# Kernel optimization log

Hardware: AMD Instinct MI355X
Metric: run time of the kernel (lower is better)

Reference implementation:

```python
import jax, jax.numpy as jnp
import numpy as np

D_IN = 768
D_OUT = 768
NUM_HEADS = 12
HEAD_DIM = D_OUT // NUM_HEADS


def setup_inputs() -> dict:
    key = jax.random.key(0)
    ks = jax.random.split(key, 6)
    s = 0.02
    x = jax.random.normal(ks[0], (4, 1024, D_IN), dtype=jnp.float32)
    # torch Linear weights are [out_features, in_features]
    Wq = jax.random.normal(ks[1], (D_OUT, D_IN), dtype=jnp.float32) * s
    Wk = jax.random.normal(ks[2], (D_OUT, D_IN), dtype=jnp.float32) * s
    Wv = jax.random.normal(ks[3], (D_OUT, D_IN), dtype=jnp.float32) * s
    Wo = jax.random.normal(ks[4], (D_OUT, D_OUT), dtype=jnp.float32) * s
    bo = jax.random.normal(ks[5], (D_OUT,), dtype=jnp.float32) * s
    return {"x": x, "Wq": Wq, "Wk": Wk, "Wv": Wv, "Wo": Wo, "bo": bo}


def reference(x, Wq, Wk, Wv, Wo, bo):
    B, T, _ = x.shape
    H, Dh = NUM_HEADS, HEAD_DIM
    # QKV projections (no bias), reshape to [B, H, T, Dh]
    q = (x @ Wq.T).reshape(B, T, H, Dh).transpose(0, 2, 1, 3)
    k = (x @ Wk.T).reshape(B, T, H, Dh).transpose(0, 2, 1, 3)
    v = (x @ Wv.T).reshape(B, T, H, Dh).transpose(0, 2, 1, 3)
    # Scores [B, H, T, T]. NOTE: original torch code's masked_fill and dropout
    # are not in-place / not assigned, so neither affects the output.
    scores = jnp.einsum("bhqd,bhkd->bhqk", q, k)
    attn = jax.nn.softmax(scores / np.sqrt(Dh).astype(np.float32), axis=-1)
    ctx = jnp.einsum("bhqk,bhkd->bhqd", attn, v)
    ctx = ctx.transpose(0, 2, 1, 3).reshape(B, T, H * Dh)
    return ctx @ Wo.T + bo
```

## Files before the change

kernel.cpp:

```cpp
#include <hip/hip_runtime.h>

typedef _Float16 half8 __attribute__((ext_vector_type(8)));
typedef float f32x4 __attribute__((ext_vector_type(4)));
typedef unsigned short u16;

#define NHEAD 12
#define DHEAD 64
#define DM    768
#define TSEQ  1024
#define LOG2E 1.44269504f

static constexpr size_t OFF_XH  = 0;
static constexpr size_t OFF_WQH = 3145728;
static constexpr size_t OFF_WKH = 3735552;
static constexpr size_t OFF_WVH = 4325376;
static constexpr size_t OFF_WOH = 4915200;
static constexpr size_t OFF_Q   = 5505024;
static constexpr size_t OFF_K   = 8650752;
static constexpr size_t OFF_VT  = 11796480;
static constexpr size_t OFF_CTX = 0;
static constexpr size_t OFF_OP  = 14942208;
static constexpr size_t OFF_ML_BYTES = 42467328;
static constexpr size_t WS_NEED_SPLITK = 43253760;

typedef const __attribute__((address_space(1))) void* gas_ptr;
typedef __attribute__((address_space(3))) void* las_ptr;
__device__ __forceinline__ void gload16(const _Float16* g, _Float16* l) {
    __builtin_amdgcn_global_load_lds((gas_ptr)g, (las_ptr)l, 16, 0, 0);
}

template <int CTRL>
__device__ __forceinline__ float dpp_rotf(float x) {
    int r = __builtin_amdgcn_update_dpp(0, __builtin_bit_cast(int, x), CTRL, 0xF, 0xF, true);
    return __builtin_bit_cast(float, r);
}
__device__ __forceinline__ float row16_max(float x) {
    x = fmaxf(x, dpp_rotf<0x121>(x));
    x = fmaxf(x, dpp_rotf<0x122>(x));
    x = fmaxf(x, dpp_rotf<0x124>(x));
    x = fmaxf(x, dpp_rotf<0x128>(x));
    return x;
}
__device__ __forceinline__ float row16_add(float x) {
    x = x + dpp_rotf<0x121>(x);
    x = x + dpp_rotf<0x122>(x);
    x = x + dpp_rotf<0x124>(x);
    x = x + dpp_rotf<0x128>(x);
    return x;
}

__global__ void cvt_kernel(const float* __restrict__ x, const float* __restrict__ wq,
                           const float* __restrict__ wk, const float* __restrict__ wv,
                           const float* __restrict__ wo, _Float16* __restrict__ ws) {
    int i = (blockIdx.x * 256 + threadIdx.x) * 8;
    const float* src;
    if (i < 3145728)      src = x  + i;
    else if (i < 3735552) src = wq + (i - 3145728);
    else if (i < 4325376) src = wk + (i - 3735552);
    else if (i < 4915200) src = wv + (i - 4325376);
    else                  src = wo + (i - 4915200);
    float4 v0 = *(const float4*)(src);
    float4 v1 = *(const float4*)(src + 4);
    half8 o;
    o[0] = (_Float16)v0.x; o[1] = (_Float16)v0.y;
    o[2] = (_Float16)v0.z; o[3] = (_Float16)v0.w;
    o[4] = (_Float16)v1.x; o[5] = (_Float16)v1.y;
    o[6] = (_Float16)v1.z; o[7] = (_Float16)v1.w;
    *(half8*)(ws + i) = o;
}

__global__ __launch_bounds__(256) void qkv_kernel(_Float16* __restrict__ ws) {
    __shared__ __align__(16) _Float16 ldsA[2][128 * 64];
    __shared__ __align__(16) _Float16 ldsB[2][128 * 64];

    const int z = blockIdx.z;
    const _Float16* __restrict__ xh = ws + OFF_XH;
    const _Float16* __restrict__ w  = ws + (z == 0 ? OFF_WQH : z == 1 ? OFF_WKH : OFF_WVH);
    _Float16* __restrict__ outp     = ws + (z == 0 ? OFF_Q   : z == 1 ? OFF_K   : OFF_VT);

    const int tid  = threadIdx.x;
    const int lane = tid & 63;
    const int wid  = tid >> 6;
    const int quad = lane >> 4, l15 = lane & 15;
    const int wm = (wid & 1) * 64, wn = (wid >> 1) * 64;

    int mb, nb;
    const _Float16 *gA, *gB;
    if (z < 2) {
        mb = blockIdx.x * 128;
        nb = blockIdx.y * 128;
        gA = xh + (size_t)mb * DM;
        gB = w  + (size_t)nb * DM;
    } else {
        mb = blockIdx.y * 128;
        nb = blockIdx.x * 128;
        gA = w  + (size_t)mb * DM;
        gB = xh + (size_t)nb * DM;
    }

    const int srow = tid >> 3;
    const int scol = (((tid & 7) ^ (srow & 7)) * 8);

    auto stage = [&](int buf, int k0) {
#pragma unroll
        for (int c = 0; c < 4; c++) {
            gload16(gA + (size_t)(c * 32 + srow) * DM + scol + k0, &ldsA[buf][c * 2048 + wid * 512]);
            gload16(gB + (size_t)(c * 32 + srow) * DM + scol + k0, &ldsB[buf][c * 2048 + wid * 512]);
        }
    };

    f32x4 acc[4][4] = {};
    stage(0, 0);
    __syncthreads();
    int cur = 0;
    for (int k0 = 0; k0 < DM; k0 += 64) {
        if (k0 + 64 < DM) stage(cur ^ 1, k0 + 64);
        const _Float16* lA = ldsA[cur];
        const _Float16* lB = ldsB[cur];
#pragma unroll
        for (int ks = 0; ks < 2; ks++) {
            half8 a[4], b[4];
#pragma unroll
            for (int t = 0; t < 4; t++) {
                const int phys = (((ks * 4 + quad) ^ (l15 & 7)) * 8);
                a[t] = *(const half8*)(lA + (wm + t * 16 + l15) * 64 + phys);
                b[t] = *(const half8*)(lB + (wn + t * 16 + l15) * 64 + phys);
            }
#pragma unroll
            for (int mt = 0; mt < 4; mt++)
#pragma unroll
                for (int nt = 0; nt < 4; nt++)
                    acc[mt][nt] = __builtin_amdgcn_mfma_f32_16x16x32_f16(a[mt], b[nt], acc[mt][nt], 0, 0, 0);
        }
        __syncthreads();
        cur ^= 1;
    }

#pragma unroll
    for (int mt = 0; mt < 4; mt++)
#pragma unroll
        for (int nt = 0; nt < 4; nt++)
#pragma unroll
            for (int r = 0; r < 4; r++) {
                int m = mb + wm + mt * 16 + quad * 4 + r;
                int n = nb + wn + nt * 16 + l15;
                size_t idx;
                if (z < 2) {
                    int bb = m >> 10, tt = m & 1023;
                    int h = n >> 6, d = n & 63;
                    idx = ((size_t)(bb * NHEAD + h) * TSEQ + tt) * DHEAD + d;
                } else {
                    int h = m >> 6, d = m & 63;
                    int bb = n >> 10, tt = n & 1023;
                    idx = ((size_t)(bb * NHEAD + h) * DHEAD + d) * TSEQ + tt;
                }
                outp[idx] = (_Float16)acc[mt][nt][r];
            }
}

template <int NZ>
__device__ __forceinline__ void attn_body(_Float16* __restrict__ ws) {
    __shared__ __align__(16) _Float16 ldsK[64 * 64];
    __shared__ __align__(16) _Float16 ldsV[64 * 64];
    __shared__ __align__(16) _Float16 ldsP[4][16 * 72];

    const int tid  = threadIdx.x;
    const int lane = tid & 63;
    const int wid  = tid >> 6;
    const int quad = lane >> 4, l15 = lane & 15;
    const int bh = blockIdx.y;
    const int z  = (NZ > 1) ? blockIdx.z : 0;
    const int q0 = blockIdx.x * 64 + wid * 16;
    const int kbeg = z * (TSEQ / NZ), kend = kbeg + TSEQ / NZ;

    const _Float16* __restrict__ Q  = ws + OFF_Q  + (size_t)bh * TSEQ * DHEAD;
    const _Float16* __restrict__ K  = ws + OFF_K  + (size_t)bh * TSEQ * DHEAD;
    const _Float16* __restrict__ VT = ws + OFF_VT + (size_t)bh * DHEAD * TSEQ;
    _Float16* pbase = ldsP[wid];

    const int srow0 = tid >> 3, sc0 = tid & 7;
    const int ldsOff0 = srow0 * 64 + ((sc0 ^ (srow0 & 7)) * 8);
    const int ldsOff1 = (srow0 + 32) * 64 + ((sc0 ^ (srow0 & 7)) * 8);

    half8 qf[2];
#pragma unroll
    for (int ks = 0; ks < 2; ks++) {
        qf[ks] = *(const half8*)(Q + (size_t)(q0 + l15) * DHEAD + ks * 32 + quad * 8);
        qf[ks] = qf[ks] * (_Float16)0.125f;
    }

    float mrun[4], lrun[4];
    f32x4 oacc[4] = {};
#pragma unroll
    for (int r = 0; r < 4; r++) { mrun[r] = -1e30f; lrun[r] = 0.f; }

    uint4 ka, kb, va, vb;
    ka = *(const uint4*)(K + kbeg * DHEAD + tid * 8);
    kb = *(const uint4*)(K + kbeg * DHEAD + 2048 + tid * 8);
    va = *(const uint4*)(VT + (size_t)srow0 * TSEQ + kbeg + sc0 * 8);
    vb = *(const uint4*)(VT + (size_t)(srow0 + 32) * TSEQ + kbeg + sc0 * 8);

    for (int kt = kbeg; kt < kend; kt += 64) {
        *(uint4*)(ldsK + ldsOff0) = ka;
        *(uint4*)(ldsK + ldsOff1) = kb;
        *(uint4*)(ldsV + ldsOff0) = va;
        *(uint4*)(ldsV + ldsOff1) = vb;
        __syncthreads();

        if (kt + 64 < kend) {
            ka = *(const uint4*)(K + (kt + 64) * DHEAD + tid * 8);
            kb = *(const uint4*)(K + (kt + 64) * DHEAD + 2048 + tid * 8);
            va = *(const uint4*)(VT + (size_t)srow0 * TSEQ + kt + 64 + sc0 * 8);
            vb = *(const uint4*)(VT + (size_t)(srow0 + 32) * TSEQ + kt + 64 + sc0 * 8);
        }

        half8 kf[4][2];
#pragma unroll
        for (int n = 0; n < 4; n++)
#pragma unroll
            for (int ks = 0; ks < 2; ks++) {
                int row = n * 16 + l15;
                int phys = (ks * 4 + quad) ^ (row & 7);
                kf[n][ks] = *(const half8*)(ldsK + row * 64 + phys * 8);
            }

        f32x4 s[4] = {};
#pragma unroll
        for (int n = 0; n < 4; n++)
#pragma unroll
            for (int ks = 0; ks < 2; ks++)
                s[n] = __builtin_amdgcn_mfma_f32_16x16x32_f16(qf[ks], kf[n][ks], s[n], 0, 0, 0);

        float tm[4];
#pragma unroll
        for (int r = 0; r < 4; r++) {
            float t = fmaxf(fmaxf(s[0][r], s[1][r]), fmaxf(s[2][r], s[3][r]));
            tm[r] = row16_max(t);
        }
        float need = fmaxf(fmaxf(tm[0] - mrun[0], tm[1] - mrun[1]),
                           fmaxf(tm[2] - mrun[2], tm[3] - mrun[3]));
        if (!__all(need <= 4.0f)) {
#pragma unroll
            for (int r = 0; r < 4; r++) {
                float mnew = fmaxf(mrun[r], tm[r]);
                float alpha = __builtin_amdgcn_exp2f((mrun[r] - mnew) * LOG2E);
                mrun[r] = mnew;
                lrun[r] *= alpha;
#pragma unroll
                for (int dn = 0; dn < 4; dn++) oacc[dn][r] *= alpha;
            }
        }
#pragma unroll
        for (int r = 0; r < 4; r++) {
            float mL = mrun[r] * LOG2E;
            float ts = 0.f;
#pragma unroll
            for (int n = 0; n < 4; n++) {
                float e = __builtin_amdgcn_exp2f(__builtin_fmaf(s[n][r], LOG2E, -mL));
                s[n][r] = e;
                ts += e;
            }
            ts = row16_add(ts);
            lrun[r] += ts;
        }

#pragma unroll
        for (int n = 0; n < 4; n++)
#pragma unroll
            for (int r = 0; r < 4; r++)
                pbase[(quad * 4 + r) * 72 + n * 16 + l15] = (_Float16)s[n][r];

        half8 vf[4][2];
#pragma unroll
        for (int dn = 0; dn < 4; dn++)
#pragma unroll
            for (int ks = 0; ks < 2; ks++) {
                int row = dn * 16 + l15;
                int phys = (ks * 4 + quad) ^ (row & 7);
                vf[dn][ks] = *(const half8*)(ldsV + row * 64 + phys * 8);
            }

        half8 pf[2];
#pragma unroll
        for (int ks = 0; ks < 2; ks++)
            pf[ks] = *(const half8*)(pbase + l15 * 72 + ks * 32 + quad * 8);

#pragma unroll
        for (int dn = 0; dn < 4; dn++)
#pragma unroll
            for (int ks = 0; ks < 2; ks++)
                oacc[dn] = __builtin_amdgcn_mfma_f32_16x16x32_f16(pf[ks], vf[dn][ks], oacc[dn], 0, 0, 0);

        __syncthreads();
    }

    if (NZ == 1) {
        _Float16* __restrict__ ctx = ws + OFF_CTX;
        const int b_ = bh / NHEAD, h = bh % NHEAD;
#pragma unroll
        for (int dn = 0; dn < 4; dn++)
#pragma unroll
            for (int r = 0; r < 4; r++) {
                int t_ = q0 + quad * 4 + r;
                int col = h * DHEAD + dn * 16 + l15;
                float v = oacc[dn][r] / lrun[r];
                ctx[((size_t)(b_ * TSEQ + t_)) * DM + col] = (_Float16)v;
            }
    } else {
        _Float16* __restrict__ op = ws + OFF_OP;
        float* __restrict__ ml = (float*)((char*)ws + OFF_ML_BYTES);
        const size_t rowbase = (size_t)z * 48 * TSEQ + (size_t)bh * TSEQ + q0;
#pragma unroll
        for (int dn = 0; dn < 4; dn++)
#pragma unroll
            for (int r = 0; r < 4; r++) {
                size_t row = rowbase + quad * 4 + r;
                op[row * 64 + dn * 16 + l15] = (_Float16)oacc[dn][r];
            }
        if (l15 == 0) {
#pragma unroll
            for (int r = 0; r < 4; r++) {
                size_t row = rowbase + quad * 4 + r;
                ml[row * 2]     = mrun[r];
                ml[row * 2 + 1] = lrun[r];
            }
        }
    }
}

__global__ __launch_bounds__(256, 3) void attn_kernel(_Float16* __restrict__ ws) {
    attn_body<1>(ws);
}
__global__ __launch_bounds__(256, 4) void attn_splitk_kernel(_Float16* __restrict__ ws) {
    attn_body<2>(ws);
}

__global__ __launch_bounds__(256) void combine_kernel(_Float16* __restrict__ ws) {
    const _Float16* __restrict__ op = ws + OFF_OP;
    const float* __restrict__ ml = (const float*)((const char*)ws + OFF_ML_BYTES);
    _Float16* __restrict__ ctx = ws + OFF_CTX;

    int g = blockIdx.x * 256 + threadIdx.x;
    int row = g >> 3, chunk = g & 7;
    int bh = row >> 10, q = row & 1023;
    int b_ = bh / NHEAD, h = bh % NHEAD;

    float m0 = ml[(size_t)row * 2], l0 = ml[(size_t)row * 2 + 1];
    float m1 = ml[(size_t)(49152 + row) * 2], l1 = ml[(size_t)(49152 + row) * 2 + 1];
    float M = fmaxf(m0, m1);
    float w0 = __builtin_amdgcn_exp2f((m0 - M) * LOG2E);
    float w1 = __builtin_amdgcn_exp2f((m1 - M) * LOG2E);
    float inv_l = 1.0f / (w0 * l0 + w1 * l1);

    half8 o0 = *(const half8*)(op + (size_t)row * 64 + chunk * 8);
    half8 o1 = *(const half8*)(op + (size_t)(49152 + row) * 64 + chunk * 8);
    half8 o;
#pragma unroll
    for (int j = 0; j < 8; j++)
        o[j] = (_Float16)(((float)o0[j] * w0 + (float)o1[j] * w1) * inv_l);
    *(half8*)(ctx + ((size_t)(b_ * TSEQ + q)) * DM + h * DHEAD + chunk * 8) = o;
}

__global__ __launch_bounds__(256) void proj_kernel(const _Float16* __restrict__ ws,
                                                   const float* __restrict__ bo,
                                                   float* __restrict__ out) {
    __shared__ __align__(16) _Float16 ldsA[2][64 * 64];
    __shared__ __align__(16) _Float16 ldsB[2][64 * 64];

    const _Float16* __restrict__ gA = ws + OFF_CTX + (size_t)blockIdx.x * 64 * DM;
    const _Float16* __restrict__ gB = ws + OFF_WOH + (size_t)blockIdx.y * 64 * DM;

    const int tid  = threadIdx.x;
    const int lane = tid & 63;
    const int wid  = tid >> 6;
    const int quad = lane >> 4, l15 = lane & 15;
    const int wm = (wid & 1) * 32, wn = (wid >> 1) * 32;

    const int srow = tid >> 3;
    const int scol = (((tid & 7) ^ (srow & 7)) * 8);

    auto stage = [&](int buf, int k0) {
#pragma unroll
        for (int c = 0; c < 2; c++) {
            gload16(gA + (size_t)(c * 32 + srow) * DM + scol + k0, &ldsA[buf][c * 2048 + wid * 512]);
            gload16(gB + (size_t)(c * 32 + srow) * DM + scol + k0, &ldsB[buf][c * 2048 + wid * 512]);
        }
    };

    f32x4 acc[2][2] = {};
    stage(0, 0);
    __syncthreads();
    int cur = 0;
    for (int k0 = 0; k0 < DM; k0 += 64) {
        if (k0 + 64 < DM) stage(cur ^ 1, k0 + 64);
        const _Float16* lA = ldsA[cur];
        const _Float16* lB = ldsB[cur];
#pragma unroll
        for (int ks = 0; ks < 2; ks++) {
            half8 a[2], b[2];
#pragma unroll
            for (int t = 0; t < 2; t++) {
                const int phys = (((ks * 4 + quad) ^ (l15 & 7)) * 8);
                a[t] = *(const half8*)(lA + (wm + t * 16 + l15) * 64 + phys);
                b[t] = *(const half8*)(lB + (wn + t * 16 + l15) * 64 + phys);
            }
#pragma unroll
            for (int mt = 0; mt < 2; mt++)
#pragma unroll
                for (int nt = 0; nt < 2; nt++)
                    acc[mt][nt] = __builtin_amdgcn_mfma_f32_16x16x32_f16(a[mt], b[nt], acc[mt][nt], 0, 0, 0);
        }
        __syncthreads();
        cur ^= 1;
    }

    const int mb = blockIdx.x * 64, nb = blockIdx.y * 64;
#pragma unroll
    for (int mt = 0; mt < 2; mt++)
#pragma unroll
        for (int nt = 0; nt < 2; nt++)
#pragma unroll
            for (int r = 0; r < 4; r++) {
                int m = mb + wm + mt * 16 + quad * 4 + r;
                int n = nb + wn + nt * 16 + l15;
                out[(size_t)m * DM + n] = acc[mt][nt][r] + bo[n];
            }
}

extern "C" void kernel_launch(void* const* d_in, const int* in_sizes, int n_in,
                              void* d_out, int out_size, void* d_ws, size_t ws_size,
                              hipStream_t stream) {
    const float* x  = (const float*)d_in[0];
    const float* wq = (const float*)d_in[1];
    const float* wk = (const float*)d_in[2];
    const float* wv = (const float*)d_in[3];
    const float* wo = (const float*)d_in[4];
    const float* bo = (const float*)d_in[5];
    _Float16* ws = (_Float16*)d_ws;
    float* out = (float*)d_out;

    cvt_kernel<<<dim3(2688, 1, 1), 256, 0, stream>>>(x, wq, wk, wv, wo, ws);
    qkv_kernel<<<dim3(32, 6, 3), 256, 0, stream>>>(ws);
    if (ws_size >= WS_NEED_SPLITK) {
        attn_splitk_kernel<<<dim3(16, 48, 2), 256, 0, stream>>>(ws);
        combine_kernel<<<dim3(1536, 1, 1), 256, 0, stream>>>(ws);
    } else {
        attn_kernel<<<dim3(16, 48, 1), 256, 0, stream>>>(ws);
    }
    proj_kernel<<<dim3(64, 12, 1), 256, 0, stream>>>(ws, bo, out);
}
```

Before: 151.5 us.

## Process two 16-row query groups per wave to reuse K/V fragments

Each wave now handles 32 query rows instead of 16, so every K and V fragment loaded from shared memory feeds two MFMAs. The block covers 128 queries and the grid is halved, which amortises the K/V global loads and LDS staging over twice the work. The cost is more registers (launch bounds lowered to 2 blocks per SM), a larger P buffer, and fewer blocks (768 for split-K), which may reduce occupancy and latency hiding.

```diff
diff --git a/kernel.cpp b/kernel.cpp
--- a/kernel.cpp
+++ b/kernel.cpp
@@ -162,7 +162,7 @@
 __device__ __forceinline__ void attn_body(_Float16* __restrict__ ws) {
     __shared__ __align__(16) _Float16 ldsK[64 * 64];
     __shared__ __align__(16) _Float16 ldsV[64 * 64];
-    __shared__ __align__(16) _Float16 ldsP[4][16 * 72];
+    __shared__ __align__(16) _Float16 ldsP[4][32 * 72];
 
     const int tid  = threadIdx.x;
     const int lane = tid & 63;
@@ -170,7 +170,7 @@
     const int quad = lane >> 4, l15 = lane & 15;
     const int bh = blockIdx.y;
     const int z  = (NZ > 1) ? blockIdx.z : 0;
-    const int q0 = blockIdx.x * 64 + wid * 16;
+    const int q0 = blockIdx.x * 128 + wid * 32;
     const int kbeg = z * (TSEQ / NZ), kend = kbeg + TSEQ / NZ;
 
     const _Float16* __restrict__ Q  = ws + OFF_Q  + (size_t)bh * TSEQ * DHEAD;
@@ -182,17 +182,21 @@
     const int ldsOff0 = srow0 * 64 + ((sc0 ^ (srow0 & 7)) * 8);
     const int ldsOff1 = (srow0 + 32) * 64 + ((sc0 ^ (srow0 & 7)) * 8);
 
-    half8 qf[2];
-#pragma unroll
-    for (int ks = 0; ks < 2; ks++) {
-        qf[ks] = *(const half8*)(Q + (size_t)(q0 + l15) * DHEAD + ks * 32 + quad * 8);
-        qf[ks] = qf[ks] * (_Float16)0.125f;
-    }
-
-    float mrun[4], lrun[4];
-    f32x4 oacc[4] = {};
-#pragma unroll
-    for (int r = 0; r < 4; r++) { mrun[r] = -1e30f; lrun[r] = 0.f; }
+    half8 qf[2][2];
+#pragma unroll
+    for (int rg = 0; rg < 2; rg++)
+#pragma unroll
+        for (int ks = 0; ks < 2; ks++) {
+            qf[rg][ks] = *(const half8*)(Q + (size_t)(q0 + rg * 16 + l15) * DHEAD + ks * 32 + quad * 8);
+            qf[rg][ks] = qf[rg][ks] * (_Float16)0.125f;
+        }
+
+    float mrun[2][4], lrun[2][4];
+    f32x4 oacc[2][4] = {};
+#pragma unroll
+    for (int rg = 0; rg < 2; rg++)
+#pragma unroll
+        for (int r = 0; r < 4; r++) { mrun[rg][r] = -1e30f; lrun[rg][r] = 0.f; }
 
     uint4 ka, kb, va, vb;
     ka = *(const uint4*)(K + kbeg * DHEAD + tid * 8);
@@ -224,51 +228,65 @@
                 kf[n][ks] = *(const half8*)(ldsK + row * 64 + phys * 8);
             }
 
-        f32x4 s[4] = {};
+        f32x4 s[2][4] = {};
 #pragma unroll
         for (int n = 0; n < 4; n++)
 #pragma unroll
             for (int ks = 0; ks < 2; ks++)
-                s[n] = __builtin_amdgcn_mfma_f32_16x16x32_f16(qf[ks], kf[n][ks], s[n], 0, 0, 0);
-
-        float tm[4];
-#pragma unroll
-        for (int r = 0; r < 4; r++) {
-            float t = fmaxf(fmaxf(s[0][r], s[1][r]), fmaxf(s[2][r], s[3][r]));
-            tm[r] = row16_max(t);
-        }
-        float need = fmaxf(fmaxf(tm[0] - mrun[0], tm[1] - mrun[1]),
-                           fmaxf(tm[2] - mrun[2], tm[3] - mrun[3]));
+#pragma unroll
+                for (int rg = 0; rg < 2; rg++)
+                    s[rg][n] = __builtin_amdgcn_mfma_f32_16x16x32_f16(qf[rg][ks], kf[n][ks], s[rg][n], 0, 0, 0);
+
+        float tm[2][4];
+#pragma unroll
+        for (int rg = 0; rg < 2; rg++)
+#pragma unroll
+            for (int r = 0; r < 4; r++) {
+                float t = fmaxf(fmaxf(s[rg][0][r], s[rg][1][r]), fmaxf(s[rg][2][r], s[rg][3][r]));
+                tm[rg][r] = row16_max(t);
+            }
+        float need = -1e30f;
+#pragma unroll
+        for (int rg = 0; rg < 2; rg++)
+#pragma unroll
+            for (int r = 0; r < 4; r++)
+                need = fmaxf(need, tm[rg][r] - mrun[rg][r]);
         if (!__all(need <= 4.0f)) {
 #pragma unroll
+            for (int rg = 0; rg < 2; rg++)
+#pragma unroll
+                for (int r = 0; r < 4; r++) {
+                    float mnew = fmaxf(mrun[rg][r], tm[rg][r]);
+                    float alpha = __builtin_amdgcn_exp2f((mrun[rg][r] - mnew) * LOG2E);
+                    mrun[rg][r] = mnew;
+                    lrun[rg][r] *= alpha;
+#pragma unroll
+                    for (int dn = 0; dn < 4; dn++) oacc[rg][dn][r] *= alpha;
+                }
+        }
+#pragma unroll
+        for (int rg = 0; rg < 2; rg++)
+#pragma unroll
             for (int r = 0; r < 4; r++) {
-                float mnew = fmaxf(mrun[r], tm[r]);
-                float alpha = __builtin_amdgcn_exp2f((mrun[r] - mnew) * LOG2E);
-                mrun[r] = mnew;
-                lrun[r] *= alpha;
-#pragma unroll
-                for (int dn = 0; dn < 4; dn++) oacc[dn][r] *= alpha;
-            }
-        }
-#pragma unroll
-        for (int r = 0; r < 4; r++) {
-            float mL = mrun[r] * LOG2E;
-            float ts = 0.f;
-#pragma unroll
-            for (int n = 0; n < 4; n++) {
-                float e = __builtin_amdgcn_exp2f(__builtin_fmaf(s[n][r], LOG2E, -mL));
-                s[n][r] = e;
-                ts += e;
-            }
-            ts = row16_add(ts);
-            lrun[r] += ts;
-        }
-
-#pragma unroll
-        for (int n = 0; n < 4; n++)
-#pragma unroll
-            for (int r = 0; r < 4; r++)
-                pbase[(quad * 4 + r) * 72 + n * 16 + l15] = (_Float16)s[n][r];
+                float mL = mrun[rg][r] * LOG2E;
+                float ts = 0.f;
+#pragma unroll
+                for (int n = 0; n < 4; n++) {
+                    float e = __builtin_amdgcn_exp2f(__builtin_fmaf(s[rg][n][r], LOG2E, -mL));
+                    s[rg][n][r] = e;
+                    ts += e;
+                }
+                ts = row16_add(ts);
+                lrun[rg][r] += ts;
+            }
+
+#pragma unroll
+        for (int rg = 0; rg < 2; rg++)
+#pragma unroll
+            for (int n = 0; n < 4; n++)
+#pragma unroll
+                for (int r = 0; r < 4; r++)
+                    pbase[(rg * 16 + quad * 4 + r) * 72 + n * 16 + l15] = (_Float16)s[rg][n][r];
 
         half8 vf[4][2];
 #pragma unroll
@@ -280,16 +298,20 @@
                 vf[dn][ks] = *(const half8*)(ldsV + row * 64 + phys * 8);
             }
 
-        half8 pf[2];
-#pragma unroll
-        for (int ks = 0; ks < 2; ks++)
-            pf[ks] = *(const half8*)(pbase + l15 * 72 + ks * 32 + quad * 8);
+        half8 pf[2][2];
+#pragma unroll
+        for (int rg = 0; rg < 2; rg++)
+#pragma unroll
+            for (int ks = 0; ks < 2; ks++)
+                pf[rg][ks] = *(const half8*)(pbase + (rg * 16 + l15) * 72 + ks * 32 + quad * 8);
 
 #pragma unroll
         for (int dn = 0; dn < 4; dn++)
 #pragma unroll
             for (int ks = 0; ks < 2; ks++)
-                oacc[dn] = __builtin_amdgcn_mfma_f32_16x16x32_f16(pf[ks], vf[dn][ks], oacc[dn], 0, 0, 0);
+#pragma unroll
+                for (int rg = 0; rg < 2; rg++)
+                    oacc[rg][dn] = __builtin_amdgcn_mfma_f32_16x16x32_f16(pf[rg][ks], vf[dn][ks], oacc[rg][dn], 0, 0, 0);
 
         __syncthreads();
     }
@@ -298,40 +320,46 @@
         _Float16* __restrict__ ctx = ws + OFF_CTX;
         const int b_ = bh / NHEAD, h = bh % NHEAD;
 #pragma unroll
-        for (int dn = 0; dn < 4; dn++)
-#pragma unroll
-            for (int r = 0; r < 4; r++) {
-                int t_ = q0 + quad * 4 + r;
-                int col = h * DHEAD + dn * 16 + l15;
-                float v = oacc[dn][r] / lrun[r];
-                ctx[((size_t)(b_ * TSEQ + t_)) * DM + col] = (_Float16)v;
-            }
+        for (int rg = 0; rg < 2; rg++)
+#pragma unroll
+            for (int dn = 0; dn < 4; dn++)
+#pragma unroll
+                for (int r = 0; r < 4; r++) {
+                    int t_ = q0 + rg * 16 + quad * 4 + r;
+                    int col = h * DHEAD + dn * 16 + l15;
+                    float v = oacc[rg][dn][r] / lrun[rg][r];
+                    ctx[((size_t)(b_ * TSEQ + t_)) * DM + col] = (_Float16)v;
+                }
     } else {
         _Float16* __restrict__ op = ws + OFF_OP;
         float* __restrict__ ml = (float*)((char*)ws + OFF_ML_BYTES);
         const size_t rowbase = (size_t)z * 48 * TSEQ + (size_t)bh * TSEQ + q0;
 #pragma unroll
-        for (int dn = 0; dn < 4; dn++)
-#pragma unroll
-            for (int r = 0; r < 4; r++) {
-                size_t row = rowbase + quad * 4 + r;
-                op[row * 64 + dn * 16 + l15] = (_Float16)oacc[dn][r];
-            }
+        for (int rg = 0; rg < 2; rg++)
+#pragma unroll
+            for (int dn = 0; dn < 4; dn++)
+#pragma unroll
+                for (int r = 0; r < 4; r++) {
+                    size_t row = rowbase + rg * 16 + quad * 4 + r;
+                    op[row * 64 + dn * 16 + l15] = (_Float16)oacc[rg][dn][r];
+                }
         if (l15 == 0) {
 #pragma unroll
-            for (int r = 0; r < 4; r++) {
-                size_t row = rowbase + quad * 4 + r;
-                ml[row * 2]     = mrun[r];
-                ml[row * 2 + 1] = lrun[r];
-            }
-        }
-    }
-}
-
-__global__ __launch_bounds__(256, 3) void attn_kernel(_Float16* __restrict__ ws) {
+            for (int rg = 0; rg < 2; rg++)
+#pragma unroll
+                for (int r = 0; r < 4; r++) {
+                    size_t row = rowbase + rg * 16 + quad * 4 + r;
+                    ml[row * 2]     = mrun[rg][r];
+                    ml[row * 2 + 1] = lrun[rg][r];
+                }
+        }
+    }
+}
+
+__global__ __launch_bounds__(256, 2) void attn_kernel(_Float16* __restrict__ ws) {
     attn_body<1>(ws);
 }
-__global__ __launch_bounds__(256, 4) void attn_splitk_kernel(_Float16* __restrict__ ws) {
+__global__ __launch_bounds__(256, 2) void attn_splitk_kernel(_Float16* __restrict__ ws) {
     attn_body<2>(ws);
 }
 
@@ -442,10 +470,10 @@
     cvt_kernel<<<dim3(2688, 1, 1), 256, 0, stream>>>(x, wq, wk, wv, wo, ws);
     qkv_kernel<<<dim3(32, 6, 3), 256, 0, stream>>>(ws);
     if (ws_size >= WS_NEED_SPLITK) {
-        attn_splitk_kernel<<<dim3(16, 48, 2), 256, 0, stream>>>(ws);
+        attn_splitk_kernel<<<dim3(8, 48, 2), 256, 0, stream>>>(ws);
         combine_kernel<<<dim3(1536, 1, 1), 256, 0, stream>>>(ws);
     } else {
-        attn_kernel<<<dim3(16, 48, 1), 256, 0, stream>>>(ws);
+        attn_kernel<<<dim3(8, 48, 1), 256, 0, stream>>>(ws);
     }
     proj_kernel<<<dim3(64, 12, 1), 256, 0, stream>>>(ws, bo, out);
 }
```

Result: no change. 149.2 us (-1.5%).
